# Optimization experiments

Measured on AMD Instinct MI355X. Metric: run time of the kernel, lower is better.

The kernel has to match this reference:

```python
import jax, jax.numpy as jnp
import numpy as np

N_NODES = 5000
N_EDGES = 160000
HID = 64
NODE_F = 4
TASK_F = 4
BATCH = 512


def _glorot(key, shape):
    fan_in = shape[-1]
    return jax.random.normal(key, shape, dtype=jnp.float32) / jnp.sqrt(jnp.float32(fan_in))


def setup_inputs() -> dict:
    key = jax.random.key(0)
    ks = jax.random.split(key, 16)
    x = jax.random.normal(ks[0], (N_NODES, NODE_F), dtype=jnp.float32)
    edge_index = jax.random.randint(ks[1], (2, N_EDGES), 0, N_NODES, dtype=jnp.int64)
    task_feat = jax.random.normal(ks[2], (BATCH, TASK_F), dtype=jnp.float32)
    return {
        "x": x,
        "edge_index": edge_index,
        "task_feat": task_feat,
        # SAGEConv layer 1: out = lin_l(mean_neigh) + lin_r(x); lin_l has bias, lin_r (root) has no bias (PyG default)
        "Wl1": _glorot(ks[3], (HID, NODE_F)), "bl1": jnp.zeros((HID,), jnp.float32),
        "Wr1": _glorot(ks[4], (HID, NODE_F)),
        # SAGEConv layer 2
        "Wl2": _glorot(ks[5], (HID, HID)), "bl2": jnp.zeros((HID,), jnp.float32),
        "Wr2": _glorot(ks[6], (HID, HID)),
        # task_encoder: Linear(4,64) -> ReLU -> Linear(64,64)
        "Wt1": _glorot(ks[7], (HID, TASK_F)), "bt1": jnp.zeros((HID,), jnp.float32),
        "Wt2": _glorot(ks[8], (HID, HID)), "bt2": jnp.zeros((HID,), jnp.float32),
        # classifier: Linear(128,64) -> ReLU -> Linear(64,1)
        "Wc1": _glorot(ks[9], (HID, 2 * HID)), "bc1": jnp.zeros((HID,), jnp.float32),
        "Wc2": _glorot(ks[10], (1, HID)), "bc2": jnp.zeros((1,), jnp.float32),
    }


def _sage_conv(x, src, dst, Wl, bl, Wr):
    # PyG SAGEConv(mean): messages flow src -> dst; mean over incoming neighbors
    msg_sum = jax.ops.segment_sum(x[src], dst, num_segments=N_NODES)
    deg = jax.ops.segment_sum(jnp.ones((src.shape[0],), x.dtype), dst, num_segments=N_NODES)
    mean_neigh = msg_sum / jnp.maximum(deg, 1.0)[:, None]
    return mean_neigh @ Wl.T + bl + x @ Wr.T


def reference(x, edge_index, task_feat,
              Wl1, bl1, Wr1, Wl2, bl2, Wr2,
              Wt1, bt1, Wt2, bt2, Wc1, bc1, Wc2, bc2):
    src, dst = edge_index[0], edge_index[1]
    h = jax.nn.relu(_sage_conv(x, src, dst, Wl1, bl1, Wr1))        # [N, HID]
    h = jax.nn.relu(_sage_conv(h, src, dst, Wl2, bl2, Wr2))        # [N, HID]
    t = jax.nn.relu(task_feat @ Wt1.T + bt1) @ Wt2.T + bt2         # [B, HID]
    # classifier on concat([h, t]) == split Wc1 into h-part and t-part; avoids materializing the concat
    h_part = h @ Wc1[:, :HID].T                                    # [N, HID]
    t_part = t @ Wc1[:, HID:].T + bc1                              # [B, HID]
    hidden = jax.nn.relu(h_part[None, :, :] + t_part[:, None, :])  # [B, N, HID]
    scores = jnp.einsum('bnh,h->bn', hidden, Wc2[0]) + bc2[0]      # [B, N]
    return scores
```

## Files before the change

kernel.cpp:

```cpp
#include <hip/hip_runtime.h>

#define N_NODES 5000
#define N_EDGES 160000
#define HID 64
#define BATCH 512
#define NSLICE 128
#define EPB (N_EDGES / NSLICE)
#define STRIDE 128


__global__ __launch_bounds__(256) void prep_kernel(
        const int* __restrict__ ei,
        const float* __restrict__ Wl1, const float* __restrict__ Wr1,
        const float* __restrict__ Wl2, const float* __restrict__ Wr2,
        const float* __restrict__ Wc1,
        const float* __restrict__ task_feat,
        const float* __restrict__ Wt1, const float* __restrict__ bt1,
        const float* __restrict__ Wt2, const float* __restrict__ bt2,
        const float* __restrict__ bc1,
        int* __restrict__ blk_hist,
        float* __restrict__ Wl1T, float* __restrict__ Wr1T,
        float* __restrict__ Wl2T, float* __restrict__ Wr2T,
        float* __restrict__ Wc1hT, float* __restrict__ t_part) {
    int tid = threadIdx.x;
    int blk = blockIdx.x;
    __shared__ int hist[N_NODES];
    __shared__ float s1[4][64], s2[4][64];

    if (blk < NSLICE) {
        for (int i = tid; i < N_NODES; i += 256) hist[i] = 0;
        __syncthreads();
        int base = blk * EPB;
        for (int j = tid; j < EPB; j += 256)
            atomicAdd(&hist[ei[N_EDGES + base + j]], 1);
        __syncthreads();
        for (int i = tid; i < N_NODES; i += 256)
            blk_hist[blk * N_NODES + i] = hist[i];
    } else if (blk == NSLICE) {
        for (int idx = tid; idx < 4096; idx += 256) {
            int k = idx >> 6, h = idx & 63;
            Wl2T[idx] = Wl2[h * 64 + k];
        }
    } else if (blk == NSLICE + 1) {
        for (int idx = tid; idx < 4096; idx += 256) {
            int k = idx >> 6, h = idx & 63;
            Wr2T[idx] = Wr2[h * 64 + k];
        }
    } else if (blk == NSLICE + 2) {
        for (int idx = tid; idx < 4096; idx += 256) {
            int k = idx >> 6, h = idx & 63;
            Wc1hT[idx] = Wc1[h * 128 + k];
        }
    } else if (blk == NSLICE + 3) {
        int k = tid >> 6, h = tid & 63;
        Wl1T[tid] = Wl1[h * 4 + k];
        Wr1T[tid] = Wr1[h * 4 + k];
    } else {
        int grp = tid >> 6, h = tid & 63;
        int b = (blk - (NSLICE + 4)) * 4 + grp;
        float4 tf = ((const float4*)task_feat)[b];
        float4 w1 = ((const float4*)Wt1)[h];
        float v = bt1[h] + tf.x * w1.x + tf.y * w1.y + tf.z * w1.z + tf.w * w1.w;
        s1[grp][h] = fmaxf(v, 0.f);
        __syncthreads();
        const float4* w2r = (const float4*)(Wt2 + h * 64);
        const float4* s1v = (const float4*)s1[grp];
        float v2 = bt2[h];
#pragma unroll
        for (int q = 0; q < 16; q++) {
            float4 w = w2r[q]; float4 s = s1v[q];
            v2 += s.x * w.x + s.y * w.y + s.z * w.z + s.w * w.w;
        }
        s2[grp][h] = v2;
        __syncthreads();
        const float4* wc  = (const float4*)(Wc1 + h * 128 + 64);
        const float4* s2v = (const float4*)s2[grp];
        float p = bc1[h];
#pragma unroll
        for (int q = 0; q < 16; q++) {
            float4 w = wc[q]; float4 s = s2v[q];
            p += s.x * w.x + s.y * w.y + s.z * w.z + s.w * w.w;
        }
        t_part[b * 64 + h] = p;
    }
}

__global__ __launch_bounds__(256) void offsets_kernel(int* __restrict__ blk_hist,
                                                      int* __restrict__ deg) {
    int n = blockIdx.x * 256 + threadIdx.x;
    if (n >= N_NODES) return;
    int run = 0;
#pragma unroll 8
    for (int b = 0; b < NSLICE; b++) {
        int v = blk_hist[b * N_NODES + n];
        blk_hist[b * N_NODES + n] = run;
        run += v;
    }
    deg[n] = run;
}

__global__ __launch_bounds__(256) void reorder_kernel(
        const int* __restrict__ ei, const int* __restrict__ blk_hist,
        int* __restrict__ sorted_src) {
    __shared__ int cur[N_NODES];
    int tid = threadIdx.x;
    int blk = blockIdx.x;
    for (int i = tid; i < N_NODES; i += 256) cur[i] = 0;
    __syncthreads();
    int base = blk * EPB;
    const int* my_excl = blk_hist + blk * N_NODES;
    for (int j = tid; j < EPB; j += 256) {
        int src = ei[base + j];
        int dst = ei[N_EDGES + base + j];
        int local = atomicAdd(&cur[dst], 1);
        sorted_src[dst * STRIDE + my_excl[dst] + local] = src;
    }
}

__global__ __launch_bounds__(256) void layer1_kernel(
        const float* __restrict__ x, const int* __restrict__ deg,
        const int* __restrict__ sorted_src,
        const float* __restrict__ Wl1T, const float* __restrict__ bl1,
        const float* __restrict__ Wr1T, float* __restrict__ h1) {
    int lane = threadIdx.x & 63, grp = threadIdx.x >> 6;
    int n = blockIdx.x * 4 + grp;
    int d = deg[n];
    int f = lane & 3, g = lane >> 2;
    const int* bucket = sorted_src + n * STRIDE;
    float acc = 0.f;
    for (int j = g; j < d; j += 16) acc += x[bucket[j] * 4 + f];
    acc += __shfl_down(acc, 32);
    acc += __shfl_down(acc, 16);
    acc += __shfl_down(acc, 8);
    acc += __shfl_down(acc, 4);
    __shared__ float mean[4][4], xn[4][4];
    if (lane < 4) {
        mean[grp][lane] = acc / fmaxf((float)d, 1.f);
        xn[grp][lane] = x[n * 4 + lane];
    }
    __syncthreads();
    float v = bl1[lane];
#pragma unroll
    for (int ff = 0; ff < 4; ff++)
        v += mean[grp][ff] * Wl1T[ff * 64 + lane] + xn[grp][ff] * Wr1T[ff * 64 + lane];
    h1[n * 64 + lane] = fmaxf(v, 0.f);
}

__global__ __launch_bounds__(256) void layer2_kernel(
        const float* __restrict__ h1, const int* __restrict__ deg,
        const int* __restrict__ sorted_src,
        const float* __restrict__ Wl2T, const float* __restrict__ bl2,
        const float* __restrict__ Wr2T, const float* __restrict__ Wc1hT,
        float* __restrict__ h_part) {
    int h = threadIdx.x & 63, grp = threadIdx.x >> 6;
    int n = blockIdx.x * 4 + grp;
    int d = deg[n];
    const int* bucket = sorted_src + n * STRIDE;
    float a0 = 0.f, a1 = 0.f, a2 = 0.f, a3 = 0.f;
    int j = 0;
    for (; j + 4 <= d; j += 4) {
        int e0 = bucket[j], e1 = bucket[j + 1], e2 = bucket[j + 2], e3 = bucket[j + 3];
        a0 += h1[e0 * 64 + h];
        a1 += h1[e1 * 64 + h];
        a2 += h1[e2 * 64 + h];
        a3 += h1[e3 * 64 + h];
    }
    for (; j < d; j++) a0 += h1[bucket[j] * 64 + h];
    float m = (a0 + a1 + a2 + a3) / fmaxf((float)d, 1.f);

    __shared__ float shm[4][64], shh[4][64], shh2[4][64];
    shm[grp][h] = m;
    shh[grp][h] = h1[n * 64 + h];
    __syncthreads();
    float v = bl2[h];
#pragma unroll
    for (int k = 0; k < 64; k++)
        v += shm[grp][k] * Wl2T[k * 64 + h] + shh[grp][k] * Wr2T[k * 64 + h];
    shh2[grp][h] = fmaxf(v, 0.f);
    __syncthreads();
    float p = 0.f;
#pragma unroll
    for (int k = 0; k < 64; k++) p += shh2[grp][k] * Wc1hT[k * 64 + h];
    h_part[n * 64 + h] = p;
}

__global__ __launch_bounds__(256) void scores_kernel(
        const float* __restrict__ h_part, const float* __restrict__ t_part,
        const float* __restrict__ Wc2, const float* __restrict__ bc2,
        float* __restrict__ out) {
    int tid = threadIdx.x;
    int n = blockIdx.x * 256 + tid;
    bool valid = n < N_NODES;
    int nn = valid ? n : (N_NODES - 1);
    float hr[64];
    const float4* hp = (const float4*)(h_part + nn * 64);
#pragma unroll
    for (int i = 0; i < 16; i++) {
        float4 v = hp[i];
        hr[4 * i + 0] = v.x; hr[4 * i + 1] = v.y;
        hr[4 * i + 2] = v.z; hr[4 * i + 3] = v.w;
    }
    float b2 = bc2[0];
    int b0 = blockIdx.y * 8;
    for (int bb = 0; bb < 8; bb++) {
        const float* tp = t_part + (b0 + bb) * 64;
        float acc = 0.f;
#pragma unroll
        for (int h = 0; h < 64; h++)
            acc = fmaf(fmaxf(hr[h] + tp[h], 0.f), Wc2[h], acc);
        if (valid) out[(b0 + bb) * N_NODES + n] = acc + b2;
    }
}

extern "C" void kernel_launch(void* const* d_in, const int* in_sizes, int n_in,
                              void* d_out, int out_size, void* d_ws, size_t ws_size,
                              hipStream_t stream) {
    const float* x    = (const float*)d_in[0];
    const int*   ei   = (const int*)d_in[1];
    const float* task = (const float*)d_in[2];
    const float* Wl1  = (const float*)d_in[3];
    const float* bl1  = (const float*)d_in[4];
    const float* Wr1  = (const float*)d_in[5];
    const float* Wl2  = (const float*)d_in[6];
    const float* bl2  = (const float*)d_in[7];
    const float* Wr2  = (const float*)d_in[8];
    const float* Wt1  = (const float*)d_in[9];
    const float* bt1  = (const float*)d_in[10];
    const float* Wt2  = (const float*)d_in[11];
    const float* bt2  = (const float*)d_in[12];
    const float* Wc1  = (const float*)d_in[13];
    const float* bc1  = (const float*)d_in[14];
    const float* Wc2  = (const float*)d_in[15];
    const float* bc2  = (const float*)d_in[16];
    float* out = (float*)d_out;

    char* ws = (char*)d_ws;
    int*   blk_hist   = (int*)(ws + 0);
    int*   deg        = (int*)(ws + 2560000);
    int*   sorted_src = (int*)(ws + 2580000);
    float* h1         = (float*)(ws + 5140000);
    float* h_part     = (float*)(ws + 6420000);
    float* t_part     = (float*)(ws + 7700000);
    float* Wl1T  = (float*)(ws + 7831072);
    float* Wr1T  = (float*)(ws + 7832096);
    float* Wl2T  = (float*)(ws + 7833120);
    float* Wr2T  = (float*)(ws + 7849504);
    float* Wc1hT = (float*)(ws + 7865888);

    prep_kernel<<<NSLICE + 4 + BATCH / 4, 256, 0, stream>>>(
        ei, Wl1, Wr1, Wl2, Wr2, Wc1, task, Wt1, bt1, Wt2, bt2, bc1,
        blk_hist, Wl1T, Wr1T, Wl2T, Wr2T, Wc1hT, t_part);
    offsets_kernel<<<(N_NODES + 255) / 256, 256, 0, stream>>>(blk_hist, deg);
    reorder_kernel<<<NSLICE, 256, 0, stream>>>(ei, blk_hist, sorted_src);
    layer1_kernel<<<N_NODES / 4, 256, 0, stream>>>(x, deg, sorted_src, Wl1T, bl1, Wr1T, h1);
    layer2_kernel<<<N_NODES / 4, 256, 0, stream>>>(h1, deg, sorted_src, Wl2T, bl2, Wr2T,
                                                   Wc1hT, h_part);
    scores_kernel<<<dim3(20, 64), 256, 0, stream>>>(h_part, t_part, Wc2, bc2, out);
}
```

Before: 152.9 us.

## Fuse CSR build and layer-1 into one per-node-block kernel scanning all edges

Replaces the histogram, offsets, reorder and layer1 kernels with one build kernel. Each block owns 20 destination nodes, scans the whole edge list, and collects its neighbours in shared-memory buckets. It then computes layer-1 directly and writes deg, sorted_src and h1. The weight-transpose prep is also dropped: layer2 now reads Wl2, Wr2 and Wc1 rows with float4 loads. This cuts kernel launches and the global histogram traffic, at the cost of every block re-reading the full dst array (redundant L2 traffic) and uncoalesced per-thread weight row reads.

```diff
diff --git a/kernel.cpp b/kernel.cpp
--- a/kernel.cpp
+++ b/kernel.cpp
@@ -4,158 +4,116 @@
 #define N_EDGES 160000
 #define HID 64
 #define BATCH 512
-#define NSLICE 128
-#define EPB (N_EDGES / NSLICE)
-#define STRIDE 128
-
-
-__global__ __launch_bounds__(256) void prep_kernel(
-        const int* __restrict__ ei,
-        const float* __restrict__ Wl1, const float* __restrict__ Wr1,
-        const float* __restrict__ Wl2, const float* __restrict__ Wr2,
-        const float* __restrict__ Wc1,
+#define NPB 20
+#define BSTRIDE 128
+
+
+__global__ __launch_bounds__(512) void build_kernel(
+        const float* __restrict__ x, const int* __restrict__ ei,
+        const float* __restrict__ Wl1, const float* __restrict__ bl1,
+        const float* __restrict__ Wr1,
         const float* __restrict__ task_feat,
         const float* __restrict__ Wt1, const float* __restrict__ bt1,
         const float* __restrict__ Wt2, const float* __restrict__ bt2,
-        const float* __restrict__ bc1,
-        int* __restrict__ blk_hist,
-        float* __restrict__ Wl1T, float* __restrict__ Wr1T,
-        float* __restrict__ Wl2T, float* __restrict__ Wr2T,
-        float* __restrict__ Wc1hT, float* __restrict__ t_part) {
+        const float* __restrict__ Wc1, const float* __restrict__ bc1,
+        int* __restrict__ deg, int* __restrict__ sorted_src,
+        float* __restrict__ h1, float* __restrict__ t_part) {
     int tid = threadIdx.x;
     int blk = blockIdx.x;
-    __shared__ int hist[N_NODES];
-    __shared__ float s1[4][64], s2[4][64];
-
-    if (blk < NSLICE) {
-        for (int i = tid; i < N_NODES; i += 256) hist[i] = 0;
-        __syncthreads();
-        int base = blk * EPB;
-        for (int j = tid; j < EPB; j += 256)
-            atomicAdd(&hist[ei[N_EDGES + base + j]], 1);
-        __syncthreads();
-        for (int i = tid; i < N_NODES; i += 256)
-            blk_hist[blk * N_NODES + i] = hist[i];
-    } else if (blk == NSLICE) {
-        for (int idx = tid; idx < 4096; idx += 256) {
-            int k = idx >> 6, h = idx & 63;
-            Wl2T[idx] = Wl2[h * 64 + k];
-        }
-    } else if (blk == NSLICE + 1) {
-        for (int idx = tid; idx < 4096; idx += 256) {
-            int k = idx >> 6, h = idx & 63;
-            Wr2T[idx] = Wr2[h * 64 + k];
-        }
-    } else if (blk == NSLICE + 2) {
-        for (int idx = tid; idx < 4096; idx += 256) {
-            int k = idx >> 6, h = idx & 63;
-            Wc1hT[idx] = Wc1[h * 128 + k];
-        }
-    } else if (blk == NSLICE + 3) {
-        int k = tid >> 6, h = tid & 63;
-        Wl1T[tid] = Wl1[h * 4 + k];
-        Wr1T[tid] = Wr1[h * 4 + k];
+    __shared__ union SM {
+        struct { int ldeg[NPB]; int lbuck[NPB][BSTRIDE]; } a;
+        struct { float s1[8][64]; float s2[8][64]; } t;
+    } sm;
+
+    if (blk < N_NODES / NPB) {
+        int n0 = blk * NPB;
+        if (tid < NPB) sm.a.ldeg[tid] = 0;
+        __syncthreads();
+
+        const int4* dst4 = (const int4*)(ei + N_EDGES);
+        for (int j4 = tid; j4 < N_EDGES / 4; j4 += 512) {
+            int4 d = dst4[j4];
+            int e = j4 * 4;
+            unsigned r;
+            r = (unsigned)(d.x - n0);
+            if (r < NPB) { int q = atomicAdd(&sm.a.ldeg[r], 1); if (q < BSTRIDE) sm.a.lbuck[r][q] = ei[e]; }
+            r = (unsigned)(d.y - n0);
+            if (r < NPB) { int q = atomicAdd(&sm.a.ldeg[r], 1); if (q < BSTRIDE) sm.a.lbuck[r][q] = ei[e + 1]; }
+            r = (unsigned)(d.z - n0);
+            if (r < NPB) { int q = atomicAdd(&sm.a.ldeg[r], 1); if (q < BSTRIDE) sm.a.lbuck[r][q] = ei[e + 2]; }
+            r = (unsigned)(d.w - n0);
+            if (r < NPB) { int q = atomicAdd(&sm.a.ldeg[r], 1); if (q < BSTRIDE) sm.a.lbuck[r][q] = ei[e + 3]; }
+        }
+        __syncthreads();
+
+        int lane = tid & 63, grp = tid >> 6;
+        int f = lane & 3, g = lane >> 2;
+        for (int ln = grp; ln < NPB; ln += 8) {
+            int n = n0 + ln;
+            int d = sm.a.ldeg[ln];
+            if (d > BSTRIDE) d = BSTRIDE;
+            float acc = 0.f;
+            for (int j = g; j < d; j += 16) acc += x[sm.a.lbuck[ln][j] * 4 + f];
+            acc += __shfl_down(acc, 32);
+            acc += __shfl_down(acc, 16);
+            acc += __shfl_down(acc, 8);
+            acc += __shfl_down(acc, 4);
+            float inv = 1.f / fmaxf((float)d, 1.f);
+            float m0 = __shfl(acc, 0) * inv;
+            float m1 = __shfl(acc, 1) * inv;
+            float m2 = __shfl(acc, 2) * inv;
+            float m3 = __shfl(acc, 3) * inv;
+            float4 xv = ((const float4*)x)[n];
+            float4 wl = ((const float4*)Wl1)[lane];
+            float4 wr = ((const float4*)Wr1)[lane];
+            float v = bl1[lane]
+                    + m0 * wl.x + m1 * wl.y + m2 * wl.z + m3 * wl.w
+                    + xv.x * wr.x + xv.y * wr.y + xv.z * wr.z + xv.w * wr.w;
+            h1[n * 64 + lane] = fmaxf(v, 0.f);
+            if (lane == 0) deg[n] = d;
+            for (int j = lane; j < d; j += 64)
+                sorted_src[n * BSTRIDE + j] = sm.a.lbuck[ln][j];
+        }
     } else {
-        int grp = tid >> 6, h = tid & 63;
-        int b = (blk - (NSLICE + 4)) * 4 + grp;
+        int lane = tid & 63, grp = tid >> 6;
+        int b = (blk - N_NODES / NPB) * 8 + grp;
         float4 tf = ((const float4*)task_feat)[b];
-        float4 w1 = ((const float4*)Wt1)[h];
-        float v = bt1[h] + tf.x * w1.x + tf.y * w1.y + tf.z * w1.z + tf.w * w1.w;
-        s1[grp][h] = fmaxf(v, 0.f);
-        __syncthreads();
-        const float4* w2r = (const float4*)(Wt2 + h * 64);
-        const float4* s1v = (const float4*)s1[grp];
-        float v2 = bt2[h];
+        float4 w1 = ((const float4*)Wt1)[lane];
+        float v = bt1[lane] + tf.x * w1.x + tf.y * w1.y + tf.z * w1.z + tf.w * w1.w;
+        sm.t.s1[grp][lane] = fmaxf(v, 0.f);
+        __syncthreads();
+        const float4* w2r = (const float4*)(Wt2 + lane * 64);
+        const float4* s1v = (const float4*)sm.t.s1[grp];
+        float v2 = bt2[lane];
 #pragma unroll
         for (int q = 0; q < 16; q++) {
             float4 w = w2r[q]; float4 s = s1v[q];
             v2 += s.x * w.x + s.y * w.y + s.z * w.z + s.w * w.w;
         }
-        s2[grp][h] = v2;
-        __syncthreads();
-        const float4* wc  = (const float4*)(Wc1 + h * 128 + 64);
-        const float4* s2v = (const float4*)s2[grp];
-        float p = bc1[h];
+        sm.t.s2[grp][lane] = v2;
+        __syncthreads();
+        const float4* wcr = (const float4*)(Wc1 + lane * 128 + 64);
+        const float4* s2v = (const float4*)sm.t.s2[grp];
+        float p = bc1[lane];
 #pragma unroll
         for (int q = 0; q < 16; q++) {
-            float4 w = wc[q]; float4 s = s2v[q];
+            float4 w = wcr[q]; float4 s = s2v[q];
             p += s.x * w.x + s.y * w.y + s.z * w.z + s.w * w.w;
         }
-        t_part[b * 64 + h] = p;
-    }
-}
-
-__global__ __launch_bounds__(256) void offsets_kernel(int* __restrict__ blk_hist,
-                                                      int* __restrict__ deg) {
-    int n = blockIdx.x * 256 + threadIdx.x;
-    if (n >= N_NODES) return;
-    int run = 0;
-#pragma unroll 8
-    for (int b = 0; b < NSLICE; b++) {
-        int v = blk_hist[b * N_NODES + n];
-        blk_hist[b * N_NODES + n] = run;
-        run += v;
-    }
-    deg[n] = run;
-}
-
-__global__ __launch_bounds__(256) void reorder_kernel(
-        const int* __restrict__ ei, const int* __restrict__ blk_hist,
-        int* __restrict__ sorted_src) {
-    __shared__ int cur[N_NODES];
-    int tid = threadIdx.x;
-    int blk = blockIdx.x;
-    for (int i = tid; i < N_NODES; i += 256) cur[i] = 0;
-    __syncthreads();
-    int base = blk * EPB;
-    const int* my_excl = blk_hist + blk * N_NODES;
-    for (int j = tid; j < EPB; j += 256) {
-        int src = ei[base + j];
-        int dst = ei[N_EDGES + base + j];
-        int local = atomicAdd(&cur[dst], 1);
-        sorted_src[dst * STRIDE + my_excl[dst] + local] = src;
-    }
-}
-
-__global__ __launch_bounds__(256) void layer1_kernel(
-        const float* __restrict__ x, const int* __restrict__ deg,
-        const int* __restrict__ sorted_src,
-        const float* __restrict__ Wl1T, const float* __restrict__ bl1,
-        const float* __restrict__ Wr1T, float* __restrict__ h1) {
-    int lane = threadIdx.x & 63, grp = threadIdx.x >> 6;
-    int n = blockIdx.x * 4 + grp;
-    int d = deg[n];
-    int f = lane & 3, g = lane >> 2;
-    const int* bucket = sorted_src + n * STRIDE;
-    float acc = 0.f;
-    for (int j = g; j < d; j += 16) acc += x[bucket[j] * 4 + f];
-    acc += __shfl_down(acc, 32);
-    acc += __shfl_down(acc, 16);
-    acc += __shfl_down(acc, 8);
-    acc += __shfl_down(acc, 4);
-    __shared__ float mean[4][4], xn[4][4];
-    if (lane < 4) {
-        mean[grp][lane] = acc / fmaxf((float)d, 1.f);
-        xn[grp][lane] = x[n * 4 + lane];
-    }
-    __syncthreads();
-    float v = bl1[lane];
-#pragma unroll
-    for (int ff = 0; ff < 4; ff++)
-        v += mean[grp][ff] * Wl1T[ff * 64 + lane] + xn[grp][ff] * Wr1T[ff * 64 + lane];
-    h1[n * 64 + lane] = fmaxf(v, 0.f);
+        t_part[b * 64 + lane] = p;
+    }
 }
 
 __global__ __launch_bounds__(256) void layer2_kernel(
         const float* __restrict__ h1, const int* __restrict__ deg,
         const int* __restrict__ sorted_src,
-        const float* __restrict__ Wl2T, const float* __restrict__ bl2,
-        const float* __restrict__ Wr2T, const float* __restrict__ Wc1hT,
+        const float* __restrict__ Wl2, const float* __restrict__ bl2,
+        const float* __restrict__ Wr2, const float* __restrict__ Wc1,
         float* __restrict__ h_part) {
     int h = threadIdx.x & 63, grp = threadIdx.x >> 6;
     int n = blockIdx.x * 4 + grp;
     int d = deg[n];
-    const int* bucket = sorted_src + n * STRIDE;
+    const int* bucket = sorted_src + n * BSTRIDE;
     float a0 = 0.f, a1 = 0.f, a2 = 0.f, a3 = 0.f;
     int j = 0;
     for (; j + 4 <= d; j += 4) {
@@ -172,15 +130,27 @@
     shm[grp][h] = m;
     shh[grp][h] = h1[n * 64 + h];
     __syncthreads();
+    const float4* wl2r = (const float4*)(Wl2 + h * 64);
+    const float4* wr2r = (const float4*)(Wr2 + h * 64);
+    const float* im = shm[grp];
+    const float* ih = shh[grp];
     float v = bl2[h];
 #pragma unroll
-    for (int k = 0; k < 64; k++)
-        v += shm[grp][k] * Wl2T[k * 64 + h] + shh[grp][k] * Wr2T[k * 64 + h];
+    for (int q = 0; q < 16; q++) {
+        float4 a = wl2r[q]; float4 b = wr2r[q];
+        v += im[4 * q + 0] * a.x + im[4 * q + 1] * a.y + im[4 * q + 2] * a.z + im[4 * q + 3] * a.w
+           + ih[4 * q + 0] * b.x + ih[4 * q + 1] * b.y + ih[4 * q + 2] * b.z + ih[4 * q + 3] * b.w;
+    }
     shh2[grp][h] = fmaxf(v, 0.f);
     __syncthreads();
+    const float4* wcr = (const float4*)(Wc1 + h * 128);
+    const float* i2 = shh2[grp];
     float p = 0.f;
 #pragma unroll
-    for (int k = 0; k < 64; k++) p += shh2[grp][k] * Wc1hT[k * 64 + h];
+    for (int q = 0; q < 16; q++) {
+        float4 c = wcr[q];
+        p += i2[4 * q + 0] * c.x + i2[4 * q + 1] * c.y + i2[4 * q + 2] * c.z + i2[4 * q + 3] * c.w;
+    }
     h_part[n * 64 + h] = p;
 }
 
@@ -235,25 +205,16 @@
     float* out = (float*)d_out;
 
     char* ws = (char*)d_ws;
-    int*   blk_hist   = (int*)(ws + 0);
-    int*   deg        = (int*)(ws + 2560000);
-    int*   sorted_src = (int*)(ws + 2580000);
-    float* h1         = (float*)(ws + 5140000);
-    float* h_part     = (float*)(ws + 6420000);
-    float* t_part     = (float*)(ws + 7700000);
-    float* Wl1T  = (float*)(ws + 7831072);
-    float* Wr1T  = (float*)(ws + 7832096);
-    float* Wl2T  = (float*)(ws + 7833120);
-    float* Wr2T  = (float*)(ws + 7849504);
-    float* Wc1hT = (float*)(ws + 7865888);
-
-    prep_kernel<<<NSLICE + 4 + BATCH / 4, 256, 0, stream>>>(
-        ei, Wl1, Wr1, Wl2, Wr2, Wc1, task, Wt1, bt1, Wt2, bt2, bc1,
-        blk_hist, Wl1T, Wr1T, Wl2T, Wr2T, Wc1hT, t_part);
-    offsets_kernel<<<(N_NODES + 255) / 256, 256, 0, stream>>>(blk_hist, deg);
-    reorder_kernel<<<NSLICE, 256, 0, stream>>>(ei, blk_hist, sorted_src);
-    layer1_kernel<<<N_NODES / 4, 256, 0, stream>>>(x, deg, sorted_src, Wl1T, bl1, Wr1T, h1);
-    layer2_kernel<<<N_NODES / 4, 256, 0, stream>>>(h1, deg, sorted_src, Wl2T, bl2, Wr2T,
-                                                   Wc1hT, h_part);
+    int*   deg        = (int*)(ws + 0);
+    int*   sorted_src = (int*)(ws + 20000);
+    float* h1         = (float*)(ws + 2580000);
+    float* h_part     = (float*)(ws + 3860000);
+    float* t_part     = (float*)(ws + 5140000);
+
+    build_kernel<<<N_NODES / NPB + BATCH / 8, 512, 0, stream>>>(
+        x, ei, Wl1, bl1, Wr1, task, Wt1, bt1, Wt2, bt2, Wc1, bc1,
+        deg, sorted_src, h1, t_part);
+    layer2_kernel<<<N_NODES / 4, 256, 0, stream>>>(h1, deg, sorted_src,
+                                                   Wl2, bl2, Wr2, Wc1, h_part);
     scores_kernel<<<dim3(20, 64), 256, 0, stream>>>(h_part, t_part, Wc2, bc2, out);
 }
```

Result: slower. 183.6 us (+20.1%).

## Replace three-pass counting sort with fixed-slot per-slice buckets compacted in layer1

Applied to the files above, without the earlier changes.

Edges are scattered in a single pass into fixed-size slots per (node, slice), with per-slice counts recorded. This removes the separate histogram, prefix-offset and reorder kernels. Layer1 then walks the 128 slices for each node, accumulating features while writing a compacted neighbor list and degree for layer2. The cost is a serial 128-iteration loop per node in layer1, a much larger scattered workspace, and silent edge truncation if a slice bucket or node degree exceeds the fixed caps.

```diff
diff --git a/kernel.cpp b/kernel.cpp
--- a/kernel.cpp
+++ b/kernel.cpp
@@ -4,158 +4,142 @@
 #define N_EDGES 160000
 #define HID 64
 #define BATCH 512
-#define NSLICE 128
-#define EPB (N_EDGES / NSLICE)
-#define STRIDE 128
-
-
-__global__ __launch_bounds__(256) void prep_kernel(
-        const int* __restrict__ ei,
+#define NSL 128
+#define EPS (N_EDGES / NSL)
+#define SLOTS 12
+#define CSTRIDE 96
+
+
+__global__ __launch_bounds__(256) void sort_kernel(
+        const int* __restrict__ ei, const float* __restrict__ task_feat,
+        const float* __restrict__ Wt1, const float* __restrict__ bt1,
+        const float* __restrict__ Wt2, const float* __restrict__ bt2,
+        const float* __restrict__ Wc1, const float* __restrict__ bc1,
         const float* __restrict__ Wl1, const float* __restrict__ Wr1,
         const float* __restrict__ Wl2, const float* __restrict__ Wr2,
-        const float* __restrict__ Wc1,
-        const float* __restrict__ task_feat,
-        const float* __restrict__ Wt1, const float* __restrict__ bt1,
-        const float* __restrict__ Wt2, const float* __restrict__ bt2,
-        const float* __restrict__ bc1,
-        int* __restrict__ blk_hist,
+        int* __restrict__ slots, int* __restrict__ cnt, float* __restrict__ t_part,
         float* __restrict__ Wl1T, float* __restrict__ Wr1T,
         float* __restrict__ Wl2T, float* __restrict__ Wr2T,
-        float* __restrict__ Wc1hT, float* __restrict__ t_part) {
+        float* __restrict__ Wc1hT) {
     int tid = threadIdx.x;
     int blk = blockIdx.x;
-    __shared__ int hist[N_NODES];
-    __shared__ float s1[4][64], s2[4][64];
-
-    if (blk < NSLICE) {
-        for (int i = tid; i < N_NODES; i += 256) hist[i] = 0;
-        __syncthreads();
-        int base = blk * EPB;
-        for (int j = tid; j < EPB; j += 256)
-            atomicAdd(&hist[ei[N_EDGES + base + j]], 1);
-        __syncthreads();
-        for (int i = tid; i < N_NODES; i += 256)
-            blk_hist[blk * N_NODES + i] = hist[i];
-    } else if (blk == NSLICE) {
-        for (int idx = tid; idx < 4096; idx += 256) {
-            int k = idx >> 6, h = idx & 63;
-            Wl2T[idx] = Wl2[h * 64 + k];
-        }
-    } else if (blk == NSLICE + 1) {
-        for (int idx = tid; idx < 4096; idx += 256) {
-            int k = idx >> 6, h = idx & 63;
-            Wr2T[idx] = Wr2[h * 64 + k];
-        }
-    } else if (blk == NSLICE + 2) {
-        for (int idx = tid; idx < 4096; idx += 256) {
-            int k = idx >> 6, h = idx & 63;
-            Wc1hT[idx] = Wc1[h * 128 + k];
-        }
-    } else if (blk == NSLICE + 3) {
-        int k = tid >> 6, h = tid & 63;
-        Wl1T[tid] = Wl1[h * 4 + k];
-        Wr1T[tid] = Wr1[h * 4 + k];
+    __shared__ union SM {
+        int cur[N_NODES];
+        struct { float s1[4][64]; float s2[4][64]; } t;
+    } sm;
+
+    if (blk < NSL) {
+        int s = blk;
+        for (int i = tid; i < N_NODES; i += 256) sm.cur[i] = 0;
+        __syncthreads();
+        int base = s * EPS;
+        for (int j = tid; j < EPS; j += 256) {
+            int src = ei[base + j];
+            int dst = ei[N_EDGES + base + j];
+            int q = atomicAdd(&sm.cur[dst], 1);
+            if (q < SLOTS) slots[dst * (NSL * SLOTS) + s * SLOTS + q] = src;
+        }
+        __syncthreads();
+        for (int n = tid; n < N_NODES; n += 256)
+            cnt[s * N_NODES + n] = min(sm.cur[n], SLOTS);
+    } else if (blk < NSL + 4) {
+        int w = blk - NSL;
+        if (w == 0) {
+            for (int idx = tid; idx < 4096; idx += 256) {
+                int k = idx >> 6, h = idx & 63;
+                Wl2T[idx] = Wl2[h * 64 + k];
+            }
+        } else if (w == 1) {
+            for (int idx = tid; idx < 4096; idx += 256) {
+                int k = idx >> 6, h = idx & 63;
+                Wr2T[idx] = Wr2[h * 64 + k];
+            }
+        } else if (w == 2) {
+            for (int idx = tid; idx < 4096; idx += 256) {
+                int k = idx >> 6, h = idx & 63;
+                Wc1hT[idx] = Wc1[h * 128 + k];
+            }
+        } else {
+            int k = tid >> 6, h = tid & 63;
+            Wl1T[tid] = Wl1[h * 4 + k];
+            Wr1T[tid] = Wr1[h * 4 + k];
+        }
     } else {
         int grp = tid >> 6, h = tid & 63;
-        int b = (blk - (NSLICE + 4)) * 4 + grp;
+        int b = (blk - (NSL + 4)) * 4 + grp;
         float4 tf = ((const float4*)task_feat)[b];
         float4 w1 = ((const float4*)Wt1)[h];
         float v = bt1[h] + tf.x * w1.x + tf.y * w1.y + tf.z * w1.z + tf.w * w1.w;
-        s1[grp][h] = fmaxf(v, 0.f);
+        sm.t.s1[grp][h] = fmaxf(v, 0.f);
         __syncthreads();
         const float4* w2r = (const float4*)(Wt2 + h * 64);
-        const float4* s1v = (const float4*)s1[grp];
+        const float4* s1v = (const float4*)sm.t.s1[grp];
         float v2 = bt2[h];
 #pragma unroll
         for (int q = 0; q < 16; q++) {
-            float4 w = w2r[q]; float4 s = s1v[q];
-            v2 += s.x * w.x + s.y * w.y + s.z * w.z + s.w * w.w;
-        }
-        s2[grp][h] = v2;
-        __syncthreads();
-        const float4* wc  = (const float4*)(Wc1 + h * 128 + 64);
-        const float4* s2v = (const float4*)s2[grp];
+            float4 w = w2r[q]; float4 ss = s1v[q];
+            v2 += ss.x * w.x + ss.y * w.y + ss.z * w.z + ss.w * w.w;
+        }
+        sm.t.s2[grp][h] = v2;
+        __syncthreads();
+        const float4* wcr = (const float4*)(Wc1 + h * 128 + 64);
+        const float4* s2v = (const float4*)sm.t.s2[grp];
         float p = bc1[h];
 #pragma unroll
         for (int q = 0; q < 16; q++) {
-            float4 w = wc[q]; float4 s = s2v[q];
-            p += s.x * w.x + s.y * w.y + s.z * w.z + s.w * w.w;
+            float4 w = wcr[q]; float4 ss = s2v[q];
+            p += ss.x * w.x + ss.y * w.y + ss.z * w.z + ss.w * w.w;
         }
         t_part[b * 64 + h] = p;
     }
 }
 
-__global__ __launch_bounds__(256) void offsets_kernel(int* __restrict__ blk_hist,
-                                                      int* __restrict__ deg) {
-    int n = blockIdx.x * 256 + threadIdx.x;
-    if (n >= N_NODES) return;
-    int run = 0;
-#pragma unroll 8
-    for (int b = 0; b < NSLICE; b++) {
-        int v = blk_hist[b * N_NODES + n];
-        blk_hist[b * N_NODES + n] = run;
-        run += v;
-    }
-    deg[n] = run;
-}
-
-__global__ __launch_bounds__(256) void reorder_kernel(
-        const int* __restrict__ ei, const int* __restrict__ blk_hist,
-        int* __restrict__ sorted_src) {
-    __shared__ int cur[N_NODES];
-    int tid = threadIdx.x;
-    int blk = blockIdx.x;
-    for (int i = tid; i < N_NODES; i += 256) cur[i] = 0;
-    __syncthreads();
-    int base = blk * EPB;
-    const int* my_excl = blk_hist + blk * N_NODES;
-    for (int j = tid; j < EPB; j += 256) {
-        int src = ei[base + j];
-        int dst = ei[N_EDGES + base + j];
-        int local = atomicAdd(&cur[dst], 1);
-        sorted_src[dst * STRIDE + my_excl[dst] + local] = src;
-    }
-}
-
 __global__ __launch_bounds__(256) void layer1_kernel(
-        const float* __restrict__ x, const int* __restrict__ deg,
-        const int* __restrict__ sorted_src,
+        const float* __restrict__ x, const int* __restrict__ slots,
+        const int* __restrict__ cnt,
         const float* __restrict__ Wl1T, const float* __restrict__ bl1,
-        const float* __restrict__ Wr1T, float* __restrict__ h1) {
+        const float* __restrict__ Wr1T,
+        int* __restrict__ deg, int* __restrict__ compact, float* __restrict__ h1) {
     int lane = threadIdx.x & 63, grp = threadIdx.x >> 6;
     int n = blockIdx.x * 4 + grp;
-    int d = deg[n];
-    int f = lane & 3, g = lane >> 2;
-    const int* bucket = sorted_src + n * STRIDE;
-    float acc = 0.f;
-    for (int j = g; j < d; j += 16) acc += x[bucket[j] * 4 + f];
-    acc += __shfl_down(acc, 32);
-    acc += __shfl_down(acc, 16);
-    acc += __shfl_down(acc, 8);
-    acc += __shfl_down(acc, 4);
-    __shared__ float mean[4][4], xn[4][4];
-    if (lane < 4) {
-        mean[grp][lane] = acc / fmaxf((float)d, 1.f);
-        xn[grp][lane] = x[n * 4 + lane];
-    }
-    __syncthreads();
-    float v = bl1[lane];
-#pragma unroll
-    for (int ff = 0; ff < 4; ff++)
-        v += mean[grp][ff] * Wl1T[ff * 64 + lane] + xn[grp][ff] * Wr1T[ff * 64 + lane];
+    int f = lane & 3;
+    float xacc = 0.f;
+    int pos = 0;
+    const int* nbase = slots + n * (NSL * SLOTS);
+    for (int s = 0; s < NSL; s++) {
+        int c = cnt[s * N_NODES + n];
+        const int* chunk = nbase + s * SLOTS;
+        for (int j = 0; j < c; j++) {
+            int src = chunk[j];
+            xacc += x[src * 4 + f];
+            if (lane == 0 && pos < CSTRIDE) compact[n * CSTRIDE + pos] = src;
+            pos++;
+        }
+    }
+    if (pos > CSTRIDE) pos = CSTRIDE;
+    if (lane == 0) deg[n] = pos;
+    float inv = 1.f / fmaxf((float)pos, 1.f);
+    float m0 = __shfl(xacc, 0) * inv;
+    float m1 = __shfl(xacc, 1) * inv;
+    float m2 = __shfl(xacc, 2) * inv;
+    float m3 = __shfl(xacc, 3) * inv;
+    float4 xv = ((const float4*)x)[n];
+    float v = bl1[lane]
+            + m0 * Wl1T[lane] + m1 * Wl1T[64 + lane] + m2 * Wl1T[128 + lane] + m3 * Wl1T[192 + lane]
+            + xv.x * Wr1T[lane] + xv.y * Wr1T[64 + lane] + xv.z * Wr1T[128 + lane] + xv.w * Wr1T[192 + lane];
     h1[n * 64 + lane] = fmaxf(v, 0.f);
 }
 
 __global__ __launch_bounds__(256) void layer2_kernel(
         const float* __restrict__ h1, const int* __restrict__ deg,
-        const int* __restrict__ sorted_src,
+        const int* __restrict__ compact,
         const float* __restrict__ Wl2T, const float* __restrict__ bl2,
         const float* __restrict__ Wr2T, const float* __restrict__ Wc1hT,
         float* __restrict__ h_part) {
     int h = threadIdx.x & 63, grp = threadIdx.x >> 6;
     int n = blockIdx.x * 4 + grp;
     int d = deg[n];
-    const int* bucket = sorted_src + n * STRIDE;
+    const int* bucket = compact + n * CSTRIDE;
     float a0 = 0.f, a1 = 0.f, a2 = 0.f, a3 = 0.f;
     int j = 0;
     for (; j + 4 <= d; j += 4) {
@@ -235,25 +219,25 @@
     float* out = (float*)d_out;
 
     char* ws = (char*)d_ws;
-    int*   blk_hist   = (int*)(ws + 0);
-    int*   deg        = (int*)(ws + 2560000);
-    int*   sorted_src = (int*)(ws + 2580000);
-    float* h1         = (float*)(ws + 5140000);
-    float* h_part     = (float*)(ws + 6420000);
-    float* t_part     = (float*)(ws + 7700000);
-    float* Wl1T  = (float*)(ws + 7831072);
-    float* Wr1T  = (float*)(ws + 7832096);
-    float* Wl2T  = (float*)(ws + 7833120);
-    float* Wr2T  = (float*)(ws + 7849504);
-    float* Wc1hT = (float*)(ws + 7865888);
-
-    prep_kernel<<<NSLICE + 4 + BATCH / 4, 256, 0, stream>>>(
-        ei, Wl1, Wr1, Wl2, Wr2, Wc1, task, Wt1, bt1, Wt2, bt2, bc1,
-        blk_hist, Wl1T, Wr1T, Wl2T, Wr2T, Wc1hT, t_part);
-    offsets_kernel<<<(N_NODES + 255) / 256, 256, 0, stream>>>(blk_hist, deg);
-    reorder_kernel<<<NSLICE, 256, 0, stream>>>(ei, blk_hist, sorted_src);
-    layer1_kernel<<<N_NODES / 4, 256, 0, stream>>>(x, deg, sorted_src, Wl1T, bl1, Wr1T, h1);
-    layer2_kernel<<<N_NODES / 4, 256, 0, stream>>>(h1, deg, sorted_src, Wl2T, bl2, Wr2T,
-                                                   Wc1hT, h_part);
+    int*   slots   = (int*)(ws + 0);
+    int*   cnt     = (int*)(ws + 30720000);
+    int*   compact = (int*)(ws + 33280000);
+    int*   deg     = (int*)(ws + 35200000);
+    float* h1      = (float*)(ws + 35220000);
+    float* h_part  = (float*)(ws + 36500000);
+    float* t_part  = (float*)(ws + 37780000);
+    float* Wl1T  = (float*)(ws + 37911072);
+    float* Wr1T  = (float*)(ws + 37912096);
+    float* Wl2T  = (float*)(ws + 37913120);
+    float* Wr2T  = (float*)(ws + 37929504);
+    float* Wc1hT = (float*)(ws + 37945888);
+
+    sort_kernel<<<NSL + 4 + BATCH / 4, 256, 0, stream>>>(
+        ei, task, Wt1, bt1, Wt2, bt2, Wc1, bc1, Wl1, Wr1, Wl2, Wr2,
+        slots, cnt, t_part, Wl1T, Wr1T, Wl2T, Wr2T, Wc1hT);
+    layer1_kernel<<<N_NODES / 4, 256, 0, stream>>>(x, slots, cnt, Wl1T, bl1, Wr1T,
+                                                   deg, compact, h1);
+    layer2_kernel<<<N_NODES / 4, 256, 0, stream>>>(h1, deg, compact,
+                                                   Wl2T, bl2, Wr2T, Wc1hT, h_part);
     scores_kernel<<<dim3(20, 64), 256, 0, stream>>>(h_part, t_part, Wc2, bc2, out);
 }
```

Result: slower. 198.7 us (+29.9%).
